# Kernel tuning notes

Measured on AMD Instinct MI355X. Metric: run time of the kernel, lower is better.

The kernel has to match this reference:

```python
import jax, jax.numpy as jnp
import numpy as np
from jax import lax

EPS = 1e-5
SLOPE = 0.01  # MONAI UnetResBlock leakyrelu negative_slope


def sparsemax(z):
    # z: [B, K]
    K = z.shape[-1]
    zs = jnp.sort(z, axis=-1)[..., ::-1]              # descending
    cs = jnp.cumsum(zs, axis=-1)
    k = jnp.arange(1, K + 1, dtype=z.dtype)
    support = 1.0 + k * zs > cs                        # [B, K] bool
    kmax = jnp.sum(support, axis=-1, keepdims=True)    # [B, 1] int
    tau = (jnp.take_along_axis(cs, kmax - 1, axis=-1) - 1.0) / kmax.astype(z.dtype)
    return jnp.maximum(z - tau, 0.0)


def instnorm(x):
    m = jnp.mean(x, axis=(2, 3), keepdims=True)
    v = jnp.var(x, axis=(2, 3), keepdims=True)
    return (x - m) * lax.rsqrt(v + EPS)


def lrelu(x):
    return jnp.where(x >= 0, x, SLOPE * x)


def conv3x3(x, w):
    return lax.conv_general_dilated(x, w, (1, 1), ((1, 1), (1, 1)),
                                    dimension_numbers=('NCHW', 'OIHW', 'NCHW'))


def sparse_mix(x, Wg, bg, A):
    # SparseModule: sparsemax-gated mixture of K 1x1 convs (bias=False).
    # Instead of materializing K outputs, mix weights per-sample then apply once.
    g = sparsemax(jnp.mean(x, axis=(2, 3)) @ Wg.T + bg)   # [B, K]
    Wmix = jnp.einsum('bk,koi->boi', g, A)                # [B, O, I]
    return jnp.einsum('boi,bihw->bohw', Wmix, x)


def setup_inputs() -> dict:
    key = jax.random.key(0)
    ks = jax.random.split(key, 16)
    B, Cin, Cout, H, W, K = 16, 256, 128, 48, 48, 4
    s = 0.05
    inp = jax.random.normal(ks[0], (B, Cin, H, W), jnp.float32)
    skip = jax.random.normal(ks[1], (B, Cout, 2 * H, 2 * W), jnp.float32)
    wt = jax.random.normal(ks[2], (Cin, Cout, 2, 2), jnp.float32) * s          # ConvTranspose2d [in,out,kh,kw]
    conv1_w = jax.random.normal(ks[3], (Cout, 2 * Cout, 3, 3), jnp.float32) * s
    Wg1 = jax.random.normal(ks[4], (K, 2 * Cout), jnp.float32) * s
    bg1 = jax.random.normal(ks[5], (K,), jnp.float32) * s
    A1 = jax.random.normal(ks[6], (K, Cout, 2 * Cout), jnp.float32) * s
    conv2_w = jax.random.normal(ks[7], (Cout, Cout, 3, 3), jnp.float32) * s
    Wg2 = jax.random.normal(ks[8], (K, Cout), jnp.float32) * s
    bg2 = jax.random.normal(ks[9], (K,), jnp.float32) * s
    A2 = jax.random.normal(ks[10], (K, Cout, Cout), jnp.float32) * s
    conv3_w = jax.random.normal(ks[11], (Cout, 2 * Cout), jnp.float32) * s      # 1x1 downsample conv
    Wg3 = jax.random.normal(ks[12], (K, 2 * Cout), jnp.float32) * s
    bg3 = jax.random.normal(ks[13], (K,), jnp.float32) * s
    A3 = jax.random.normal(ks[14], (K, Cout, 2 * Cout), jnp.float32) * s
    return dict(inp=inp, skip=skip, wt=wt,
                conv1_w=conv1_w, Wg1=Wg1, bg1=bg1, A1=A1,
                conv2_w=conv2_w, Wg2=Wg2, bg2=bg2, A2=A2,
                conv3_w=conv3_w, Wg3=Wg3, bg3=bg3, A3=A3)


def reference(inp, skip, wt, conv1_w, Wg1, bg1, A1, conv2_w, Wg2, bg2, A2,
              conv3_w, Wg3, bg3, A3):
    # transp_conv: ConvTranspose2d(k=2, s=2, p=0, bias=False) == conv with
    # lhs_dilation=2, pad k-1-p=1, flipped+transposed kernel.
    w_t = jnp.flip(jnp.transpose(wt, (1, 0, 2, 3)), axis=(2, 3))  # [out,in,2,2]
    up = lax.conv_general_dilated(inp, w_t, (1, 1), ((1, 1), (1, 1)),
                                  lhs_dilation=(2, 2),
                                  dimension_numbers=('NCHW', 'OIHW', 'NCHW'))
    x = jnp.concatenate([up, skip], axis=1)              # [B, 2*Cout, 2H, 2W]

    # UnetrBlockSLA (UnetResBlock with SLA-wrapped convs), stride=1, in!=out -> downsample branch
    out = conv3x3(x, conv1_w) + sparse_mix(x, Wg1, bg1, A1)
    out = lrelu(instnorm(out))
    out = conv3x3(out, conv2_w) + sparse_mix(out, Wg2, bg2, A2)
    out = instnorm(out)
    res = jnp.einsum('oi,bihw->bohw', conv3_w, x) + sparse_mix(x, Wg3, bg3, A3)
    res = instnorm(res)
    return lrelu(out + res)
```

## Files before the change

kernel.cpp:

```cpp
#include <hip/hip_runtime.h>


#define NB   16
#define C2   256
#define C1   128
#define HO   96
#define WO   96
#define NPIX 9216
#define HI   48
#define WI   48

typedef _Float16 f16;
typedef __attribute__((ext_vector_type(8))) _Float16 f16x8;
typedef __attribute__((ext_vector_type(4))) _Float16 f16x4;
typedef __attribute__((ext_vector_type(4))) float f32x4;

#define OFF_A     0ull
#define OFF_B3    18874368ull
#define OFF_XT    28311552ull
#define OFF_W1F   47185920ull
#define OFF_WRF   49545216ull
#define OFF_XSUM  49807360ull
#define OFF_O1SUM 49811456ull
#define OFF_G1    49813504ull
#define OFF_G2    49813568ull
#define OFF_G3    49813632ull
#define OFF_STATS 49813696ull

__global__ __launch_bounds__(256) void k_up(const float* __restrict__ inp,
                                            const float* __restrict__ wt,
                                            float* __restrict__ up) {
  int b = blockIdx.y;
  int oc = blockIdx.x & 7;
  int tile = blockIdx.x >> 3;
  int i0 = (tile / 3) * 16, j0 = (tile % 3) * 16;
  int t = threadIdx.x;
  int og = t >> 6, pg = t & 63, pi = pg >> 2, pj4 = pg & 3;

  __shared__ float  s_in[16 * 272];
  __shared__ float4 s_w4[256];

  float4 acc[4][4];
#pragma unroll
  for (int j = 0; j < 4; j++)
#pragma unroll
    for (int oo = 0; oo < 4; oo++) acc[j][oo] = make_float4(0.f, 0.f, 0.f, 0.f);

  for (int cc = 0; cc < 16; ++cc) {
#pragma unroll
    for (int it = 0; it < 16; ++it) {
      int flat = it * 256 + t;
      int ci = flat >> 8, i = (flat >> 4) & 15, j = flat & 15;
      s_in[ci * 272 + i * 17 + j] =
          inp[((size_t)(b * C2 + cc * 16 + ci) * HI + (i0 + i)) * WI + (j0 + j)];
    }
    {
      int ci = t >> 4, o = t & 15;
      s_w4[ci * 16 + o] = ((const float4*)wt)[(size_t)(cc * 16 + ci) * C1 + oc * 16 + o];
    }
    __syncthreads();
#pragma unroll
    for (int ci = 0; ci < 16; ++ci) {
      float iv[4];
#pragma unroll
      for (int q = 0; q < 4; q++) iv[q] = s_in[ci * 272 + pi * 17 + pj4 * 4 + q];
#pragma unroll
      for (int oo = 0; oo < 4; oo++) {
        float4 w = s_w4[ci * 16 + og * 4 + oo];
#pragma unroll
        for (int j = 0; j < 4; j++) {
          acc[j][oo].x += iv[j] * w.x; acc[j][oo].y += iv[j] * w.y;
          acc[j][oo].z += iv[j] * w.z; acc[j][oo].w += iv[j] * w.w;
        }
      }
    }
    __syncthreads();
  }
  int orow = 2 * (i0 + pi);
#pragma unroll
  for (int oo = 0; oo < 4; oo++) {
    int o = oc * 16 + og * 4 + oo;
    float* base = up + (size_t)(b * C1 + o) * HO * WO;
#pragma unroll
    for (int j = 0; j < 4; j++) {
      int jj = j0 + pj4 * 4 + j;
      *(float2*)(base + (size_t)orow * WO + 2 * jj)       = make_float2(acc[j][oo].x, acc[j][oo].y);
      *(float2*)(base + (size_t)(orow + 1) * WO + 2 * jj) = make_float2(acc[j][oo].z, acc[j][oo].w);
    }
  }
}

__global__ __launch_bounds__(256) void k_cvt1(const float* __restrict__ up,
                                              const float* __restrict__ skip,
                                              f16* __restrict__ xt,
                                              float* __restrict__ xsum) {
  int b = blockIdx.y, r = blockIdx.x;
  int c = threadIdx.x;
  __shared__ f16 slab[96 * 256];
  const float* src = (c < C1) ? up + ((size_t)(b * C1 + c) * HO + r) * WO
                              : skip + ((size_t)(b * C1 + (c - C1)) * HO + r) * WO;
  float sum = 0.f;
#pragma unroll
  for (int j = 0; j < 96; j += 4) {
    float4 v = *(const float4*)(src + j);
    slab[(j + 0) * 256 + c] = (f16)v.x;
    slab[(j + 1) * 256 + c] = (f16)v.y;
    slab[(j + 2) * 256 + c] = (f16)v.z;
    slab[(j + 3) * 256 + c] = (f16)v.w;
    sum += v.x + v.y + v.z + v.w;
  }
  atomicAdd(&xsum[b * 256 + c], sum);
  __syncthreads();
  uint4* dstv = (uint4*)(xt + (size_t)(b * 96 + r) * 96 * 256);
  const uint4* sv = (const uint4*)slab;
#pragma unroll
  for (int i = 0; i < 12; ++i) dstv[i * 256 + threadIdx.x] = sv[i * 256 + threadIdx.x];
}

__global__ __launch_bounds__(256) void k_gate(const float* __restrict__ xs, int CI,
                                              float scale,
                                              const float* __restrict__ Wg,
                                              const float* __restrict__ bg,
                                              float* __restrict__ g) {
  int b = blockIdx.x;
  int w = threadIdx.x >> 6, lane = threadIdx.x & 63;
  float sum = 0.f;
  for (int i = lane; i < CI; i += 64) sum += xs[b * CI + i] * Wg[w * CI + i];
  for (int off = 32; off; off >>= 1) sum += __shfl_xor(sum, off);
  __shared__ float z[4];
  if (lane == 0) z[w] = sum * scale + bg[w];
  __syncthreads();
  if (threadIdx.x == 0) {
    float zz[4] = {z[0], z[1], z[2], z[3]};
    float a0 = zz[0], a1 = zz[1], a2 = zz[2], a3 = zz[3], tmp;
    if (a0 < a1) { tmp = a0; a0 = a1; a1 = tmp; }
    if (a2 < a3) { tmp = a2; a2 = a3; a3 = tmp; }
    if (a0 < a2) { tmp = a0; a0 = a2; a2 = tmp; }
    if (a1 < a3) { tmp = a1; a1 = a3; a3 = tmp; }
    if (a1 < a2) { tmp = a1; a1 = a2; a2 = tmp; }
    float cs0 = a0, cs1 = cs0 + a1, cs2 = cs1 + a2, cs3 = cs2 + a3;
    int km = (1.f + 1.f * a0 > cs0) + (1.f + 2.f * a1 > cs1) +
             (1.f + 3.f * a2 > cs2) + (1.f + 4.f * a3 > cs3);
    float csk = (km == 1) ? cs0 : (km == 2) ? cs1 : (km == 3) ? cs2 : cs3;
    float tau = (csk - 1.f) / (float)km;
#pragma unroll
    for (int k = 0; k < 4; k++) g[b * 4 + k] = fmaxf(zz[k] - tau, 0.f);
  }
}

template <int CI, int NT, bool IS1X1>
__global__ __launch_bounds__(256) void k_fold(const float* __restrict__ convw,
                                              const float* __restrict__ Amat,
                                              const float* __restrict__ gate,
                                              f16* __restrict__ wf) {
  constexpr int NCH = CI / 32;
  int g = blockIdx.x * 256 + threadIdx.x;
  int o = g & 127;
  int cig = (g >> 7) & 3;
  int rest = g >> 9;
  int tap = rest % NT;
  int rest2 = rest / NT;
  int ch = rest2 % NCH;
  int b = rest2 / NCH;
  int ci0 = ch * 32 + cig * 8;

  float gk[4];
#pragma unroll
  for (int k = 0; k < 4; k++) gk[k] = gate[b * 4 + k];

  f16 out8[8];
#pragma unroll
  for (int e = 0; e < 8; ++e) {
    int ci = ci0 + e;
    float wv;
    if (IS1X1) wv = convw[(size_t)o * CI + ci];
    else       wv = convw[((size_t)o * CI + ci) * 9 + tap];
    if (IS1X1 || tap == 4) {
#pragma unroll
      for (int k = 0; k < 4; k++) wv += gk[k] * Amat[((size_t)k * C1 + o) * CI + ci];
    }
    out8[e] = (f16)wv;
  }
  *(uint4*)(wf + (size_t)g * 8) = *(const uint4*)out8;
}

template <int CI, bool HALO, bool HALF_OUT>
__global__ __launch_bounds__(512, 2) void k_cgemm(const f16* __restrict__ xt,
                                                  const f16* __restrict__ wf,
                                                  float* __restrict__ dst,
                                                  f16* __restrict__ dsth,
                                                  float* __restrict__ ssum,
                                                  float* __restrict__ ssq) {
  constexpr int NT = HALO ? 9 : 1;
  constexpr int NCH = CI / 32;
  int b = blockIdx.z;
  int rt = blockIdx.x >> 1, ct = blockIdx.x & 1;
  int r0 = rt * 8, c0 = ct * 48;
  int tid = threadIdx.x;
  int w = tid >> 6, l = tid & 63;
  int mh = w >> 2, nq = w & 3;
  int o0w = mh * 64;
  int l15 = l & 15, l4 = l >> 4;

  __shared__ __align__(16) f16 sx[4 * 10 * 50 * 8];
  __shared__ __align__(16) f16 sw[2][4 * 129 * 8];

  f32x4 acc[4][6];
#pragma unroll
  for (int mf = 0; mf < 4; ++mf)
#pragma unroll
    for (int nf = 0; nf < 6; ++nf) acc[mf][nf] = (f32x4){0.f, 0.f, 0.f, 0.f};

  int buf = 0;
  for (int ch = 0; ch < NCH; ++ch) {
    if (HALO) {
      for (int flat = tid; flat < 2000; flat += 512) {
        int cig = flat & 3, pos = flat >> 2;
        int rr = pos / 50, cc = pos % 50;
        int gr = r0 - 1 + rr, gc = c0 - 1 + cc;
        uint4 v = make_uint4(0u, 0u, 0u, 0u);
        if (gr >= 0 && gr < 96 && gc >= 0 && gc < 96)
          v = *(const uint4*)(xt + ((size_t)(b * 96 + gr) * 96 + gc) * CI + ch * 32 + cig * 8);
        *(uint4*)(sx + ((cig * 10 + rr) * 50 + cc) * 8) = v;
      }
    } else {
      for (int flat = tid; flat < 1536; flat += 512) {
        int cig = flat & 3, pos = flat >> 2;
        int rr = 1 + pos / 48, cc = 1 + pos % 48;
        int gr = r0 + pos / 48, gc = c0 + pos % 48;
        uint4 v = *(const uint4*)(xt + ((size_t)(b * 96 + gr) * 96 + gc) * CI + ch * 32 + cig * 8);
        *(uint4*)(sx + ((cig * 10 + rr) * 50 + cc) * 8) = v;
      }
    }
    {
      const f16* src = wf + ((size_t)(b * NCH + ch) * NT + 0) * 4096;
      int cig = tid >> 7, o = tid & 127;
      *(uint4*)(sw[buf] + (cig * 129 + o) * 8) = *(const uint4*)(src + tid * 8);
    }
    __syncthreads();
    for (int tap = 0; tap < NT; ++tap) {
      if (tap + 1 < NT) {
        const f16* src = wf + ((size_t)(b * NCH + ch) * NT + tap + 1) * 4096;
        int cig = tid >> 7, o = tid & 127;
        *(uint4*)(sw[buf ^ 1] + (cig * 129 + o) * 8) = *(const uint4*)(src + tid * 8);
      }
      int dr = HALO ? tap / 3 : 1, dc = HALO ? tap % 3 : 1;
      f16x8 af[4];
#pragma unroll
      for (int mf = 0; mf < 4; ++mf)
        af[mf] = *(const f16x8*)(sw[buf] + (l4 * 129 + o0w + mf * 16 + l15) * 8);
      f16x8 bf[6];
#pragma unroll
      for (int rr2 = 0; rr2 < 2; ++rr2)
#pragma unroll
        for (int c16 = 0; c16 < 3; ++c16) {
          int lr = nq * 2 + rr2 + dr;
          int lc = c16 * 16 + l15 + dc;
          bf[rr2 * 3 + c16] = *(const f16x8*)(sx + ((l4 * 10 + lr) * 50 + lc) * 8);
        }
#pragma unroll
      for (int mf = 0; mf < 4; ++mf)
#pragma unroll
        for (int nf = 0; nf < 6; ++nf)
          acc[mf][nf] = __builtin_amdgcn_mfma_f32_16x16x32_f16(af[mf], bf[nf], acc[mf][nf], 0, 0, 0);
      __syncthreads();
      buf ^= 1;
    }
  }

#pragma unroll
  for (int mf = 0; mf < 4; ++mf) {
#pragma unroll
    for (int reg = 0; reg < 4; ++reg) {
      int o = o0w + mf * 16 + l4 * 4 + reg;
      float s = 0.f, q = 0.f;
#pragma unroll
      for (int nf = 0; nf < 6; ++nf) {
        int rr2 = nf / 3, c16 = nf % 3;
        float v = acc[mf][nf][reg];
        int gr = r0 + nq * 2 + rr2, gc = c0 + c16 * 16 + l15;
        size_t off = ((size_t)(b * C1 + o) * 96 + gr) * 96 + gc;
        if (HALF_OUT) dsth[off] = (f16)v; else dst[off] = v;
        s += v; q += v * v;
      }
#pragma unroll
      for (int m = 1; m < 16; m <<= 1) { s += __shfl_xor(s, m); q += __shfl_xor(q, m); }
      if (l15 == 0) {
        atomicAdd(&ssum[b * C1 + o], s);
        atomicAdd(&ssq[b * C1 + o], q);
      }
    }
  }
}

__global__ __launch_bounds__(256) void k_norm1x(const float* __restrict__ buf,
                                                const float* __restrict__ ssum,
                                                const float* __restrict__ ssq,
                                                f16* __restrict__ xt2,
                                                float* __restrict__ osum) {
  int b = blockIdx.y, r = blockIdx.x;
  __shared__ f16 slab[96 * 128];
  __shared__ float mtab[128], rtab[128];
  int t = threadIdx.x;
  if (t < 128) {
    float m = ssum[b * C1 + t] * (1.0f / NPIX);
    float v = ssq[b * C1 + t] * (1.0f / NPIX) - m * m;
    mtab[t] = m; rtab[t] = rsqrtf(v + 1e-5f);
  }
  __syncthreads();
  int c = t & 127, half = t >> 7;
  const float* src = buf + ((size_t)(b * C1 + c) * HO + r) * WO + half * 48;
  float m = mtab[c], ri = rtab[c], sum = 0.f;
#pragma unroll
  for (int j = 0; j < 48; j += 4) {
    float4 v = *(const float4*)(src + j);
    float x0 = (v.x - m) * ri; x0 = x0 >= 0.f ? x0 : 0.01f * x0;
    float x1 = (v.y - m) * ri; x1 = x1 >= 0.f ? x1 : 0.01f * x1;
    float x2 = (v.z - m) * ri; x2 = x2 >= 0.f ? x2 : 0.01f * x2;
    float x3 = (v.w - m) * ri; x3 = x3 >= 0.f ? x3 : 0.01f * x3;
    slab[(half * 48 + j + 0) * 128 + c] = (f16)x0;
    slab[(half * 48 + j + 1) * 128 + c] = (f16)x1;
    slab[(half * 48 + j + 2) * 128 + c] = (f16)x2;
    slab[(half * 48 + j + 3) * 128 + c] = (f16)x3;
    sum += x0 + x1 + x2 + x3;
  }
  atomicAdd(&osum[b * C1 + c], sum);
  __syncthreads();
  uint4* dstv = (uint4*)(xt2 + (size_t)(b * 96 + r) * 96 * 128);
  const uint4* sv = (const uint4*)slab;
#pragma unroll
  for (int i = 0; i < 6; ++i) dstv[i * 256 + t] = sv[i * 256 + t];
}

__global__ __launch_bounds__(256) void k_final(const float* __restrict__ b2,
                                               const f16* __restrict__ b3,
                                               const float* __restrict__ s2s,
                                               const float* __restrict__ s2q,
                                               const float* __restrict__ s3s,
                                               const float* __restrict__ s3q,
                                               float* __restrict__ out) {
  int bc = blockIdx.x;
  float m2 = s2s[bc] * (1.0f / NPIX);
  float v2 = s2q[bc] * (1.0f / NPIX) - m2 * m2;
  float r2 = rsqrtf(v2 + 1e-5f);
  float m3 = s3s[bc] * (1.0f / NPIX);
  float v3 = s3q[bc] * (1.0f / NPIX) - m3 * m3;
  float r3 = rsqrtf(v3 + 1e-5f);
  const float4* p2 = (const float4*)(b2 + (size_t)bc * NPIX);
  const f16x4* p3 = (const f16x4*)(b3 + (size_t)bc * NPIX);
  float4* po = (float4*)(out + (size_t)bc * NPIX);
#pragma unroll
  for (int it = 0; it < 9; ++it) {
    float4 a = p2[it * 256 + threadIdx.x];
    f16x4 c = p3[it * 256 + threadIdx.x];
    float* aa = (float*)&a;
#pragma unroll
    for (int u = 0; u < 4; ++u) {
      float x = (aa[u] - m2) * r2 + ((float)c[u] - m3) * r3;
      aa[u] = (x >= 0.f) ? x : 0.01f * x;
    }
    po[it * 256 + threadIdx.x] = a;
  }
}

extern "C" void kernel_launch(void* const* d_in, const int* in_sizes, int n_in,
                              void* d_out, int out_size, void* d_ws, size_t ws_size,
                              hipStream_t stream) {
  const float* inp  = (const float*)d_in[0];
  const float* skip = (const float*)d_in[1];
  const float* wt   = (const float*)d_in[2];
  const float* c1w  = (const float*)d_in[3];
  const float* Wg1  = (const float*)d_in[4];
  const float* bg1  = (const float*)d_in[5];
  const float* A1   = (const float*)d_in[6];
  const float* c2w  = (const float*)d_in[7];
  const float* Wg2  = (const float*)d_in[8];
  const float* bg2  = (const float*)d_in[9];
  const float* A2   = (const float*)d_in[10];
  const float* c3w  = (const float*)d_in[11];
  const float* Wg3  = (const float*)d_in[12];
  const float* bg3  = (const float*)d_in[13];
  const float* A3   = (const float*)d_in[14];

  float* ws = (float*)d_ws;
  float* A    = ws + OFF_A;
  f16*  B3h   = (f16*)(ws + OFF_B3);
  f16*  XT    = (f16*)(ws + OFF_XT);
  f16*  W1F   = (f16*)(ws + OFF_W1F);
  f16*  WRF   = (f16*)(ws + OFF_WRF);
  float* XSUM = ws + OFF_XSUM;
  float* O1S  = ws + OFF_O1SUM;
  float* G1   = ws + OFF_G1;
  float* G2   = ws + OFF_G2;
  float* G3   = ws + OFF_G3;
  float* S1S = ws + OFF_STATS;
  float* S1Q = S1S + 2048;
  float* S2S = S1Q + 2048;
  float* S2Q = S2S + 2048;
  float* S3S = S2Q + 2048;
  float* S3Q = S3S + 2048;

  hipMemsetAsync(XSUM, 0, (4096 + 2048 + 192 + 12288) * sizeof(float), stream);

  k_up<<<dim3(72, NB), 256, 0, stream>>>(inp, wt, A);
  k_cvt1<<<dim3(96, NB), 256, 0, stream>>>(A, skip, XT, XSUM);
  k_gate<<<NB, 256, 0, stream>>>(XSUM, C2, 1.0f / NPIX, Wg1, bg1, G1);
  k_gate<<<NB, 256, 0, stream>>>(XSUM, C2, 1.0f / NPIX, Wg3, bg3, G3);
  k_fold<256, 9, false><<<2304, 256, 0, stream>>>(c1w, A1, G1, W1F);
  k_fold<256, 1, true><<<256, 256, 0, stream>>>(c3w, A3, G3, WRF);
  k_cgemm<256, true, false><<<dim3(24, 1, NB), 512, 0, stream>>>(XT, W1F, A, nullptr, S1S, S1Q);
  k_cgemm<256, false, true><<<dim3(24, 1, NB), 512, 0, stream>>>(XT, WRF, nullptr, B3h, S3S, S3Q);
  k_norm1x<<<dim3(96, NB), 256, 0, stream>>>(A, S1S, S1Q, XT, O1S);
  k_gate<<<NB, 256, 0, stream>>>(O1S, C1, 1.0f / NPIX, Wg2, bg2, G2);
  k_fold<128, 9, false><<<1152, 256, 0, stream>>>(c2w, A2, G2, W1F);
  k_cgemm<128, true, false><<<dim3(24, 1, NB), 512, 0, stream>>>(XT, W1F, A, nullptr, S2S, S2Q);
  k_final<<<NB * C1, 256, 0, stream>>>(A, B3h, S2S, S2Q, S3S, S3Q, (float*)d_out);
}
```

Baseline: 739.7 us.

## Fuse transposed conv into MFMA kernel writing f16 channels-last directly; add dedicated 1x1 GEMM

Replaces the fp32 scalar ConvTranspose kernel and the separate conversion pass with an MFMA f16 kernel. It writes the upsampled half straight into the channels-last f16 buffer and accumulates channel sums, after pre-folding the transposed weights into f16 tap-major layout. The skip conversion now only handles the skip channels. The residual 1x1 conv now uses a dedicated lightweight MFMA GEMM kernel instead of the general 3x3 conv kernel template. This removes an fp32 round trip of the upsampled tensor and FMA-bound compute, at the cost of f16 precision in the upsample and extra launches.

```diff
diff --git a/kernel.cpp b/kernel.cpp
--- a/kernel.cpp
+++ b/kernel.cpp
@@ -20,101 +20,141 @@
 #define OFF_XT    28311552ull
 #define OFF_W1F   47185920ull
 #define OFF_WRF   49545216ull
-#define OFF_XSUM  49807360ull
-#define OFF_O1SUM 49811456ull
-#define OFF_G1    49813504ull
-#define OFF_G2    49813568ull
-#define OFF_G3    49813632ull
-#define OFF_STATS 49813696ull
-
-__global__ __launch_bounds__(256) void k_up(const float* __restrict__ inp,
-                                            const float* __restrict__ wt,
-                                            float* __restrict__ up) {
+#define OFF_WUP   49807360ull
+#define OFF_XSUM  49872896ull
+#define OFF_O1SUM 49876992ull
+#define OFF_G1    49879040ull
+#define OFF_G2    49879104ull
+#define OFF_G3    49879168ull
+#define OFF_STATS 49879232ull
+
+__global__ __launch_bounds__(256) void k_foldup(const float* __restrict__ wt,
+                                                f16* __restrict__ wup) {
+  int g8 = blockIdx.x * 256 + threadIdx.x;
+  int o = g8 & 127, cigG = (g8 >> 7) & 31, tap = g8 >> 12;
+  f16 tmp[8];
+#pragma unroll
+  for (int e = 0; e < 8; ++e)
+    tmp[e] = (f16)wt[((size_t)(cigG * 8 + e) * 128 + o) * 4 + tap];
+  *(uint4*)(wup + (size_t)g8 * 8) = *(const uint4*)tmp;
+}
+
+__global__ __launch_bounds__(512, 2) void k_upT(const float* __restrict__ inp,
+                                                const f16* __restrict__ wup,
+                                                f16* __restrict__ xt,
+                                                float* __restrict__ xsum) {
   int b = blockIdx.y;
-  int oc = blockIdx.x & 7;
-  int tile = blockIdx.x >> 3;
-  int i0 = (tile / 3) * 16, j0 = (tile % 3) * 16;
-  int t = threadIdx.x;
-  int og = t >> 6, pg = t & 63, pi = pg >> 2, pj4 = pg & 3;
-
-  __shared__ float  s_in[16 * 272];
-  __shared__ float4 s_w4[256];
-
-  float4 acc[4][4];
-#pragma unroll
-  for (int j = 0; j < 4; j++)
-#pragma unroll
-    for (int oo = 0; oo < 4; oo++) acc[j][oo] = make_float4(0.f, 0.f, 0.f, 0.f);
-
-  for (int cc = 0; cc < 16; ++cc) {
-#pragma unroll
-    for (int it = 0; it < 16; ++it) {
-      int flat = it * 256 + t;
-      int ci = flat >> 8, i = (flat >> 4) & 15, j = flat & 15;
-      s_in[ci * 272 + i * 17 + j] =
-          inp[((size_t)(b * C2 + cc * 16 + ci) * HI + (i0 + i)) * WI + (j0 + j)];
-    }
-    {
-      int ci = t >> 4, o = t & 15;
-      s_w4[ci * 16 + o] = ((const float4*)wt)[(size_t)(cc * 16 + ci) * C1 + oc * 16 + o];
+  int rt = blockIdx.x >> 1, ct = blockIdx.x & 1;
+  int i0 = rt * 4, j0 = ct * 24;
+  int tid = threadIdx.x;
+  int w = tid >> 6, l = tid & 63;
+  int t = w & 3, mh = w >> 2;
+  int di = t >> 1, dj = t & 1;
+  int o0w = mh * 64;
+  int l15 = l & 15, l4 = l >> 4;
+
+  __shared__ __align__(16) f16 sxU[4 * 96 * 8];
+  __shared__ __align__(16) f16 swU[4 * 4 * 128 * 8];
+
+  f32x4 acc[4][6];
+#pragma unroll
+  for (int mf = 0; mf < 4; ++mf)
+#pragma unroll
+    for (int nf = 0; nf < 6; ++nf) acc[mf][nf] = (f32x4){0.f, 0.f, 0.f, 0.f};
+
+  for (int ch = 0; ch < 8; ++ch) {
+    if (tid < 384) {
+      int cig = tid / 96, px = tid % 96;
+      int pi = px / 24, pj = px % 24;
+      const float* sp = inp + ((size_t)(b * 256 + ch * 32 + cig * 8) * 48 + (i0 + pi)) * 48 + (j0 + pj);
+      f16 tmp[8];
+#pragma unroll
+      for (int e = 0; e < 8; ++e) tmp[e] = (f16)sp[(size_t)e * 2304];
+      *(uint4*)(sxU + (cig * 96 + px) * 8) = *(const uint4*)tmp;
+    }
+#pragma unroll
+    for (int q = 0; q < 4; ++q) {
+      int g = q * 512 + tid;
+      int tap = g >> 9, rem = g & 511;
+      int cigl = rem >> 7, o = rem & 127;
+      *(uint4*)(swU + ((tap * 4 + cigl) * 128 + o) * 8) =
+          *(const uint4*)(wup + (((size_t)tap * 32 + ch * 4 + cigl) * 128 + o) * 8);
     }
     __syncthreads();
-#pragma unroll
-    for (int ci = 0; ci < 16; ++ci) {
-      float iv[4];
-#pragma unroll
-      for (int q = 0; q < 4; q++) iv[q] = s_in[ci * 272 + pi * 17 + pj4 * 4 + q];
-#pragma unroll
-      for (int oo = 0; oo < 4; oo++) {
-        float4 w = s_w4[ci * 16 + og * 4 + oo];
-#pragma unroll
-        for (int j = 0; j < 4; j++) {
-          acc[j][oo].x += iv[j] * w.x; acc[j][oo].y += iv[j] * w.y;
-          acc[j][oo].z += iv[j] * w.z; acc[j][oo].w += iv[j] * w.w;
-        }
-      }
-    }
+    f16x8 af[4];
+#pragma unroll
+    for (int mf = 0; mf < 4; ++mf)
+      af[mf] = *(const f16x8*)(swU + ((t * 4 + l4) * 128 + o0w + mf * 16 + l15) * 8);
+    f16x8 bf[6];
+#pragma unroll
+    for (int nf = 0; nf < 6; ++nf)
+      bf[nf] = *(const f16x8*)(sxU + (l4 * 96 + nf * 16 + l15) * 8);
+#pragma unroll
+    for (int mf = 0; mf < 4; ++mf)
+#pragma unroll
+      for (int nf = 0; nf < 6; ++nf)
+        acc[mf][nf] = __builtin_amdgcn_mfma_f32_16x16x32_f16(af[mf], bf[nf], acc[mf][nf], 0, 0, 0);
     __syncthreads();
   }
-  int orow = 2 * (i0 + pi);
-#pragma unroll
-  for (int oo = 0; oo < 4; oo++) {
-    int o = oc * 16 + og * 4 + oo;
-    float* base = up + (size_t)(b * C1 + o) * HO * WO;
-#pragma unroll
-    for (int j = 0; j < 4; j++) {
-      int jj = j0 + pj4 * 4 + j;
-      *(float2*)(base + (size_t)orow * WO + 2 * jj)       = make_float2(acc[j][oo].x, acc[j][oo].y);
-      *(float2*)(base + (size_t)(orow + 1) * WO + 2 * jj) = make_float2(acc[j][oo].z, acc[j][oo].w);
-    }
-  }
-}
-
-__global__ __launch_bounds__(256) void k_cvt1(const float* __restrict__ up,
-                                              const float* __restrict__ skip,
+
+  float osum[4][4];
+#pragma unroll
+  for (int mf = 0; mf < 4; ++mf)
+#pragma unroll
+    for (int reg = 0; reg < 4; ++reg) osum[mf][reg] = 0.f;
+#pragma unroll
+  for (int mf = 0; mf < 4; ++mf) {
+#pragma unroll
+    for (int nf = 0; nf < 6; ++nf) {
+      int px = nf * 16 + l15, pi = px / 24, pj = px % 24;
+      int R = 2 * (i0 + pi) + di, CP = 2 * (j0 + pj) + dj;
+      f16 hv[4];
+#pragma unroll
+      for (int reg = 0; reg < 4; ++reg) {
+        float v = acc[mf][nf][reg];
+        hv[reg] = (f16)v;
+        osum[mf][reg] += v;
+      }
+      *(uint2*)(xt + ((size_t)(b * 96 + R) * 96 + CP) * 256 + o0w + mf * 16 + l4 * 4) = *(const uint2*)hv;
+    }
+  }
+#pragma unroll
+  for (int mf = 0; mf < 4; ++mf)
+#pragma unroll
+    for (int reg = 0; reg < 4; ++reg) {
+      float s = osum[mf][reg];
+#pragma unroll
+      for (int m = 1; m < 16; m <<= 1) s += __shfl_xor(s, m);
+      if (l15 == 0)
+        atomicAdd(&xsum[b * 256 + o0w + mf * 16 + l4 * 4 + reg], s);
+    }
+}
+
+__global__ __launch_bounds__(256) void k_cvts(const float* __restrict__ skip,
                                               f16* __restrict__ xt,
                                               float* __restrict__ xsum) {
   int b = blockIdx.y, r = blockIdx.x;
-  int c = threadIdx.x;
-  __shared__ f16 slab[96 * 256];
-  const float* src = (c < C1) ? up + ((size_t)(b * C1 + c) * HO + r) * WO
-                              : skip + ((size_t)(b * C1 + (c - C1)) * HO + r) * WO;
+  __shared__ f16 slab[96 * 128];
+  int tthr = threadIdx.x;
+  int c = tthr & 127, half = tthr >> 7;
+  const float* src = skip + ((size_t)(b * C1 + c) * HO + r) * WO + half * 48;
   float sum = 0.f;
 #pragma unroll
-  for (int j = 0; j < 96; j += 4) {
+  for (int j = 0; j < 48; j += 4) {
     float4 v = *(const float4*)(src + j);
-    slab[(j + 0) * 256 + c] = (f16)v.x;
-    slab[(j + 1) * 256 + c] = (f16)v.y;
-    slab[(j + 2) * 256 + c] = (f16)v.z;
-    slab[(j + 3) * 256 + c] = (f16)v.w;
+    slab[(half * 48 + j + 0) * 128 + c] = (f16)v.x;
+    slab[(half * 48 + j + 1) * 128 + c] = (f16)v.y;
+    slab[(half * 48 + j + 2) * 128 + c] = (f16)v.z;
+    slab[(half * 48 + j + 3) * 128 + c] = (f16)v.w;
     sum += v.x + v.y + v.z + v.w;
   }
-  atomicAdd(&xsum[b * 256 + c], sum);
+  atomicAdd(&xsum[b * 256 + 128 + c], sum);
   __syncthreads();
-  uint4* dstv = (uint4*)(xt + (size_t)(b * 96 + r) * 96 * 256);
   const uint4* sv = (const uint4*)slab;
-#pragma unroll
-  for (int i = 0; i < 12; ++i) dstv[i * 256 + threadIdx.x] = sv[i * 256 + threadIdx.x];
+  for (int flat = tthr; flat < 1536; flat += 256) {
+    int px = flat >> 4, u = flat & 15;
+    *(uint4*)(xt + ((size_t)(b * 96 + r) * 96 + px) * 256 + 128 + u * 8) = sv[flat];
+  }
 }
 
 __global__ __launch_bounds__(256) void k_gate(const float* __restrict__ xs, int CI,
@@ -293,6 +333,81 @@
   }
 }
 
+__global__ __launch_bounds__(512, 2) void k_rgemm(const f16* __restrict__ xt,
+                                                  const f16* __restrict__ wrf,
+                                                  f16* __restrict__ dsth,
+                                                  float* __restrict__ ssum,
+                                                  float* __restrict__ ssq) {
+  int b = blockIdx.y;
+  int r0 = blockIdx.x * 2;
+  int tid = threadIdx.x;
+  int w = tid >> 6, l = tid & 63;
+  int mh = w >> 2, nq = w & 3;
+  int o0w = mh * 64;
+  int l15 = l & 15, l4 = l >> 4;
+
+  __shared__ __align__(16) f16 sxR[4 * 192 * 8];
+  __shared__ __align__(16) f16 swR[4 * 128 * 8];
+
+  f32x4 acc[4][3];
+#pragma unroll
+  for (int mf = 0; mf < 4; ++mf)
+#pragma unroll
+    for (int nf = 0; nf < 3; ++nf) acc[mf][nf] = (f32x4){0.f, 0.f, 0.f, 0.f};
+
+  for (int ch = 0; ch < 8; ++ch) {
+    for (int flat = tid; flat < 768; flat += 512) {
+      int cig = flat / 192, px = flat % 192;
+      int R = r0 + px / 96, CP = px % 96;
+      *(uint4*)(sxR + (cig * 192 + px) * 8) =
+          *(const uint4*)(xt + ((size_t)(b * 96 + R) * 96 + CP) * 256 + ch * 32 + cig * 8);
+    }
+    {
+      int cig = tid >> 7, o = tid & 127;
+      *(uint4*)(swR + (cig * 128 + o) * 8) =
+          *(const uint4*)(wrf + ((size_t)(b * 8 + ch) * 512 + cig * 128 + o) * 8);
+    }
+    __syncthreads();
+    f16x8 af[4];
+#pragma unroll
+    for (int mf = 0; mf < 4; ++mf)
+      af[mf] = *(const f16x8*)(swR + (l4 * 128 + o0w + mf * 16 + l15) * 8);
+    f16x8 bf[3];
+#pragma unroll
+    for (int nf = 0; nf < 3; ++nf)
+      bf[nf] = *(const f16x8*)(sxR + (l4 * 192 + nq * 48 + nf * 16 + l15) * 8);
+#pragma unroll
+    for (int mf = 0; mf < 4; ++mf)
+#pragma unroll
+      for (int nf = 0; nf < 3; ++nf)
+        acc[mf][nf] = __builtin_amdgcn_mfma_f32_16x16x32_f16(af[mf], bf[nf], acc[mf][nf], 0, 0, 0);
+    __syncthreads();
+  }
+
+#pragma unroll
+  for (int mf = 0; mf < 4; ++mf) {
+#pragma unroll
+    for (int reg = 0; reg < 4; ++reg) {
+      int o = o0w + mf * 16 + l4 * 4 + reg;
+      float s = 0.f, q = 0.f;
+#pragma unroll
+      for (int nf = 0; nf < 3; ++nf) {
+        float v = acc[mf][nf][reg];
+        int px = nq * 48 + nf * 16 + l15;
+        int R = r0 + px / 96, CP = px % 96;
+        dsth[((size_t)(b * C1 + o) * 96 + R) * 96 + CP] = (f16)v;
+        s += v; q += v * v;
+      }
+#pragma unroll
+      for (int m = 1; m < 16; m <<= 1) { s += __shfl_xor(s, m); q += __shfl_xor(q, m); }
+      if (l15 == 0) {
+        atomicAdd(&ssum[b * C1 + o], s);
+        atomicAdd(&ssq[b * C1 + o], q);
+      }
+    }
+  }
+}
+
 __global__ __launch_bounds__(256) void k_norm1x(const float* __restrict__ buf,
                                                 const float* __restrict__ ssum,
                                                 const float* __restrict__ ssq,
@@ -388,6 +503,7 @@
   f16*  XT    = (f16*)(ws + OFF_XT);
   f16*  W1F   = (f16*)(ws + OFF_W1F);
   f16*  WRF   = (f16*)(ws + OFF_WRF);
+  f16*  WUP   = (f16*)(ws + OFF_WUP);
   float* XSUM = ws + OFF_XSUM;
   float* O1S  = ws + OFF_O1SUM;
   float* G1   = ws + OFF_G1;
@@ -400,16 +516,17 @@
   float* S3S = S2Q + 2048;
   float* S3Q = S3S + 2048;
 
-  hipMemsetAsync(XSUM, 0, (4096 + 2048 + 192 + 12288) * sizeof(float), stream);
-
-  k_up<<<dim3(72, NB), 256, 0, stream>>>(inp, wt, A);
-  k_cvt1<<<dim3(96, NB), 256, 0, stream>>>(A, skip, XT, XSUM);
+  hipMemsetAsync(XSUM, 0, 18624 * sizeof(float), stream);
+
+  k_foldup<<<64, 256, 0, stream>>>(wt, WUP);
+  k_upT<<<dim3(24, NB), 512, 0, stream>>>(inp, WUP, XT, XSUM);
+  k_cvts<<<dim3(96, NB), 256, 0, stream>>>(skip, XT, XSUM);
   k_gate<<<NB, 256, 0, stream>>>(XSUM, C2, 1.0f / NPIX, Wg1, bg1, G1);
   k_gate<<<NB, 256, 0, stream>>>(XSUM, C2, 1.0f / NPIX, Wg3, bg3, G3);
   k_fold<256, 9, false><<<2304, 256, 0, stream>>>(c1w, A1, G1, W1F);
   k_fold<256, 1, true><<<256, 256, 0, stream>>>(c3w, A3, G3, WRF);
   k_cgemm<256, true, false><<<dim3(24, 1, NB), 512, 0, stream>>>(XT, W1F, A, nullptr, S1S, S1Q);
-  k_cgemm<256, false, true><<<dim3(24, 1, NB), 512, 0, stream>>>(XT, WRF, nullptr, B3h, S3S, S3Q);
+  k_rgemm<<<dim3(48, NB), 512, 0, stream>>>(XT, WRF, B3h, S3S, S3Q);
   k_norm1x<<<dim3(96, NB), 256, 0, stream>>>(A, S1S, S1Q, XT, O1S);
   k_gate<<<NB, 256, 0, stream>>>(O1S, C1, 1.0f / NPIX, Wg2, bg2, G2);
   k_fold<128, 9, false><<<1152, 256, 0, stream>>>(c2w, A2, G2, W1F);
```

Measured after the change: 668.0 us. 9.7% less time.
